# Optimization experiments

Measured on AMD Instinct MI355X. Metric: run time of the kernel, lower is better.

The kernel has to match this reference:

```python
import jax, jax.numpy as jnp
import numpy as np

N_HEADS, D_MODEL, D_HEAD = 16, 1024, 64
BATCH, SEQ = 8, 1024
INIT_RANGE = 0.02
IGNORE = -100000.0


def setup_inputs() -> dict:
    key = jax.random.key(0)
    ks = jax.random.split(key, 6)
    return {
        "normalized_resid_pre": jax.random.normal(ks[0], (BATCH, SEQ, D_MODEL), jnp.float32),
        "encoder_output": jax.random.normal(ks[1], (BATCH, SEQ, D_MODEL), jnp.float32),
        "Qs": jax.random.normal(ks[2], (N_HEADS, D_MODEL, D_HEAD), jnp.float32) * INIT_RANGE,
        "Qbs": jnp.zeros((N_HEADS, D_HEAD), jnp.float32),
        "Ks": jax.random.normal(ks[3], (N_HEADS, D_MODEL, D_HEAD), jnp.float32) * INIT_RANGE,
        "Kbs": jnp.zeros((N_HEADS, D_HEAD), jnp.float32),
        "Vs": jax.random.normal(ks[4], (N_HEADS, D_MODEL, D_HEAD), jnp.float32) * INIT_RANGE,
        "Vbs": jnp.zeros((N_HEADS, D_HEAD), jnp.float32),
        "O": jax.random.normal(ks[5], (N_HEADS, D_HEAD, D_MODEL), jnp.float32) * INIT_RANGE,
        "Ob": jnp.zeros((D_MODEL,), jnp.float32),
    }


def reference(normalized_resid_pre, encoder_output, Qs, Qbs, Ks, Kbs, Vs, Vbs, O, Ob):
    sqrt_d_head = np.sqrt(D_HEAD).astype(np.float32)
    # per-head projections: q,k from encoder_output, v from normalized_resid_pre
    q = jnp.einsum('bpd,hdk->bphk', encoder_output, Qs) + Qbs
    k = jnp.einsum('bpd,hdk->bphk', encoder_output, Ks) + Kbs
    v = jnp.einsum('bpd,hdk->bphk', normalized_resid_pre, Vs) + Vbs
    # [B,H,Q,K] scores, scaled then causally masked with -1e5 (not -inf)
    scores = jnp.einsum('bqhk,bmhk->bhqm', q, k) / sqrt_d_head
    causal = jnp.triu(jnp.ones((SEQ, SEQ), bool), k=1)
    scores = jnp.where(causal, jnp.float32(IGNORE), scores)
    attn = jax.nn.softmax(scores, axis=-1)
    z = jnp.einsum('bmhk,bhqm->bqhk', v, attn)
    return jnp.einsum('bqhk,hkd->bqd', z, O) + Ob
```

## Files before the change

kernel.cpp:

```cpp
#include <hip/hip_runtime.h>
#include <hip/hip_bf16.h>
#include <cstdint>
#include <cstddef>
#include <math.h>


typedef __attribute__((ext_vector_type(8))) short short8;
typedef __attribute__((ext_vector_type(4))) short short4v;
typedef __attribute__((ext_vector_type(4))) float f32x4;

#define MFMA16(A, B, C) __builtin_amdgcn_mfma_f32_16x16x32_bf16(A, B, C, 0, 0, 0)

__device__ inline short f2bs(float f) {
    __bf16 h = (__bf16)f;
    return __builtin_bit_cast(short, h);
}

typedef const __attribute__((address_space(1))) unsigned int* as1_u32p;
typedef __attribute__((address_space(3))) unsigned int* as3_u32p;

__device__ inline void gload_lds16(const void* g, void* lds_base) {
    __builtin_amdgcn_global_load_lds((as1_u32p)(uintptr_t)g,
                                     (as3_u32p)(uintptr_t)lds_base, 16, 0, 0);
}

__global__ __launch_bounds__(256) void cvt_k(const float* __restrict__ a,
                                             const float* __restrict__ b,
                                             short* __restrict__ oa,
                                             short* __restrict__ ob) {
    const int n = 8 * 1024 * 1024;
    const float* src = blockIdx.y ? b : a;
    short* dst = blockIdx.y ? ob : oa;
    for (int i = (blockIdx.x * 256 + threadIdx.x) * 8; i < n; i += gridDim.x * 256 * 8) {
        f32x4 v0 = *(const f32x4*)(src + i), v1 = *(const f32x4*)(src + i + 4);
        short8 o;
        o[0] = f2bs(v0[0]); o[1] = f2bs(v0[1]); o[2] = f2bs(v0[2]); o[3] = f2bs(v0[3]);
        o[4] = f2bs(v1[0]); o[5] = f2bs(v1[1]); o[6] = f2bs(v1[2]); o[7] = f2bs(v1[3]);
        *(short8*)(dst + i) = o;
    }
}

__global__ __launch_bounds__(256) void wtrans_k(
    const float* __restrict__ Wq, const float* __restrict__ Wk,
    const float* __restrict__ Wv, const float* __restrict__ Wo,
    short* __restrict__ TQ, short* __restrict__ TK,
    short* __restrict__ TV, short* __restrict__ TO) {
    __shared__ short tile[64][72];
    const int wsel = blockIdx.y;
    const float* in = wsel == 0 ? Wq : wsel == 1 ? Wk : wsel == 2 ? Wv : Wo;
    short* out = wsel == 0 ? TQ : wsel == 1 ? TK : wsel == 2 ? TV : TO;
    const int h = blockIdx.x >> 4, tk = blockIdx.x & 15;
    const int t = threadIdx.x;
    size_t ioff; int istr, orow0, ocol0;
    if (wsel < 3) { ioff = (size_t)h * 65536 + (size_t)tk * 64 * 64; istr = 64;   orow0 = h * 64;  ocol0 = tk * 64; }
    else          { ioff = (size_t)h * 65536 + (size_t)tk * 64;      istr = 1024; orow0 = tk * 64; ocol0 = h * 64; }
    {
        const int r = t >> 2, c0 = (t & 3) * 16;
        const float* src = in + ioff + (size_t)r * istr + c0;
#pragma unroll
        for (int j = 0; j < 4; j++) {
            f32x4 v = *(const f32x4*)(src + j * 4);
            tile[r][c0 + j * 4 + 0] = f2bs(v[0]);
            tile[r][c0 + j * 4 + 1] = f2bs(v[1]);
            tile[r][c0 + j * 4 + 2] = f2bs(v[2]);
            tile[r][c0 + j * 4 + 3] = f2bs(v[3]);
        }
    }
    __syncthreads();
    {
        const int cc = t >> 2, rb = (t & 3) * 16;
        short8 o0, o1;
#pragma unroll
        for (int j = 0; j < 8; j++) { o0[j] = tile[rb + j][cc]; o1[j] = tile[rb + 8 + j][cc]; }
        short* dst = out + (size_t)(orow0 + cc) * 1024 + ocol0 + rb;
        *(short8*)dst = o0;
        *(short8*)(dst + 8) = o1;
    }
}

template <int MODE>
__global__ __launch_bounds__(256) void gemm_bt(const short* __restrict__ A,
                                               const short* __restrict__ B,
                                               const float* __restrict__ bias,
                                               void* __restrict__ Cp) {
    constexpr int K = 1024;
    __shared__ short As[128 * 64];
    __shared__ short Bs[128 * 64];
    const int t = threadIdx.x, l = t & 63, w = t >> 6, lr = l & 15, lg = l >> 4;
    const int wm = (w >> 1) * 64, wn = (w & 1) * 64;
    const int m0 = blockIdx.x * 128, n0 = blockIdx.y * 128;
    const int sr = l >> 3, cb = l & 7;
    f32x4 acc[4][4] = {};

    for (int k0 = 0; k0 < K; k0 += 64) {
#pragma unroll
        for (int i = 0; i < 4; i++) {
            const int c = w * 4 + i, r = c * 8 + sr, cbs = cb ^ (r & 7);
            gload_lds16(A + (size_t)(m0 + r) * K + k0 + cbs * 8, &As[c * 512]);
        }
#pragma unroll
        for (int i = 0; i < 4; i++) {
            const int c = w * 4 + i, r = c * 8 + sr, cbs = cb ^ (r & 7);
            gload_lds16(B + (size_t)(n0 + r) * K + k0 + cbs * 8, &Bs[c * 512]);
        }
        __syncthreads();
#pragma unroll
        for (int kk = 0; kk < 2; kk++) {
            short8 af[4], bf[4];
#pragma unroll
            for (int mi = 0; mi < 4; mi++) {
                const int r = wm + mi * 16 + lr;
                af[mi] = *(const short8*)&As[r * 64 + ((kk * 4 + lg) ^ (r & 7)) * 8];
            }
#pragma unroll
            for (int nj = 0; nj < 4; nj++) {
                const int r = wn + nj * 16 + lr;
                bf[nj] = *(const short8*)&Bs[r * 64 + ((kk * 4 + lg) ^ (r & 7)) * 8];
            }
#pragma unroll
            for (int mi = 0; mi < 4; mi++)
#pragma unroll
                for (int nj = 0; nj < 4; nj++)
                    acc[mi][nj] = MFMA16(af[mi], bf[nj], acc[mi][nj]);
        }
        __syncthreads();
    }

#pragma unroll
    for (int mi = 0; mi < 4; mi++) {
#pragma unroll
        for (int nj = 0; nj < 4; nj++) {
            const int col = n0 + wn + nj * 16 + lr;
            const float bv = bias[col];
            if (MODE == 2) {
                const int rowb = m0 + wm + mi * 16 + lg * 4;
                const int bb = rowb >> 10, s0 = rowb & 1023;
                const int h = col >> 6, d = col & 63;
                short4v pk;
#pragma unroll
                for (int e = 0; e < 4; e++) pk[e] = f2bs(acc[mi][nj][e] + bv);
                *(short4v*)((short*)Cp + ((size_t)(bb * 16 + h) * 64 + d) * 1024 + s0) = pk;
            } else {
#pragma unroll
                for (int e = 0; e < 4; e++) {
                    const int row = m0 + wm + mi * 16 + lg * 4 + e;
                    const float val = acc[mi][nj][e] + bv;
                    if (MODE == 1) {
                        const int bb = row >> 10, s = row & 1023;
                        const int h = col >> 6, d = col & 63;
                        ((short*)Cp)[((size_t)(bb * 16 + h) * 1024 + s) * 64 + d] = f2bs(val);
                    } else {
                        ((float*)Cp)[(size_t)row * 1024 + col] = val;
                    }
                }
            }
        }
    }
}

#define ATTN_THR 11.5415603f

__device__ __forceinline__ void attn_tile(
    const short* __restrict__ Ks, const short* __restrict__ Vt,
    short (*__restrict__ Psw)[72],
    const short8* __restrict__ qf, float* __restrict__ m,
    float* __restrict__ ps, f32x4* __restrict__ acc,
    bool diag, int lr, int lg, int rowloc) {
    f32x4 sf[4];
#pragma unroll
    for (int n = 0; n < 4; n++) {
        const int rk = n * 16 + lr;
        short8 kf0 = *(const short8*)&Ks[rk * 64 + ((lg) ^ (rk & 7)) * 8];
        short8 kf1 = *(const short8*)&Ks[rk * 64 + ((4 + lg) ^ (rk & 7)) * 8];
        f32x4 s = {};
        s = MFMA16(qf[0], kf0, s);
        s = MFMA16(qf[1], kf1, s);
        sf[n] = s;
    }
    const float SC = 0.18033688f;
#pragma unroll
    for (int n = 0; n < 4; n++)
#pragma unroll
        for (int e = 0; e < 4; e++) {
            float x = sf[n][e] * SC;
            if (diag && (n * 16 + lr > rowloc + e)) x = -1e30f;
            sf[n][e] = x;
        }
    float pm[4];
#pragma unroll
    for (int e = 0; e < 4; e++)
        pm[e] = fmaxf(fmaxf(sf[0][e], sf[1][e]), fmaxf(sf[2][e], sf[3][e]));
    bool ok = true;
#pragma unroll
    for (int e = 0; e < 4; e++) ok = ok && (pm[e] <= m[e] + ATTN_THR);
    if (!__all(ok)) {
#pragma unroll
        for (int e = 0; e < 4; e++) {
            float tm = pm[e];
#pragma unroll
            for (int off = 1; off < 16; off <<= 1)
                tm = fmaxf(tm, __shfl_xor(tm, off));
            float nm = fmaxf(m[e], tm);
            float al = exp2f(m[e] - nm);
            m[e] = nm;
            ps[e] *= al;
#pragma unroll
            for (int n4 = 0; n4 < 4; n4++) acc[n4][e] *= al;
        }
    }
#pragma unroll
    for (int e = 0; e < 4; e++) {
#pragma unroll
        for (int n = 0; n < 4; n++) {
            float p = exp2f(sf[n][e] - m[e]);
            ps[e] += p;
            Psw[lg * 4 + e][n * 16 + lr] = f2bs(p);
        }
    }
#pragma unroll
    for (int c = 0; c < 2; c++) {
        short8 pf = *(const short8*)&Psw[lr][lg * 8 + c * 32];
#pragma unroll
        for (int n4 = 0; n4 < 4; n4++) {
            const int rv = n4 * 16 + lr;
            short8 vf = *(const short8*)&Vt[rv * 64 + ((lg + 4 * c) ^ (rv & 7)) * 8];
            acc[n4] = MFMA16(pf, vf, acc[n4]);
        }
    }
}

__global__ __launch_bounds__(256, 4) void attn_k(const short* __restrict__ Q,
                                                 const short* __restrict__ Kp,
                                                 const short* __restrict__ Vg,
                                                 short* __restrict__ Z) {
    __shared__ short Ks[64 * 64];
    __shared__ short Vt[64 * 64];
    __shared__ short Ps[4][16][72];
    const int t = threadIdx.x, l = t & 63, w = t >> 6, lr = l & 15, lg = l >> 4;
    const int bh = blockIdx.x;
    const int qbA = blockIdx.y, qbB = 15 - qbA;
    const int q0A = qbA * 64, q0B = qbB * 64;
    const size_t base = (size_t)bh * 65536;
    const int sr = l >> 3, cb = l & 7;
    const int rowloc = w * 16 + lg * 4;

    short8 qfA[2], qfB[2];
    {
        const short* qp = Q + base + (size_t)(q0A + w * 16 + lr) * 64 + lg * 8;
        qfA[0] = *(const short8*)qp;
        qfA[1] = *(const short8*)(qp + 32);
        qp = Q + base + (size_t)(q0B + w * 16 + lr) * 64 + lg * 8;
        qfB[0] = *(const short8*)qp;
        qfB[1] = *(const short8*)(qp + 32);
    }

    float mA[4], mB[4], psA[4], psB[4];
    f32x4 accA[4] = {}, accB[4] = {};
#pragma unroll
    for (int e = 0; e < 4; e++) { mA[e] = mB[e] = -1e30f; psA[e] = psB[e] = 0.f; }

    for (int kt = 0; kt <= qbB; kt++) {
        const int k0 = kt * 64;
#pragma unroll
        for (int i = 0; i < 2; i++) {
            const int c = w * 2 + i, r = c * 8 + sr, cbs = cb ^ (r & 7);
            gload_lds16(Kp + base + (size_t)(k0 + r) * 64 + cbs * 8, &Ks[c * 512]);
            gload_lds16(Vg + base + (size_t)r * 1024 + k0 + cbs * 8, &Vt[c * 512]);
        }
        __syncthreads();
        if (kt <= qbA)
            attn_tile(Ks, Vt, Ps[w], qfA, mA, psA, accA, kt == qbA, lr, lg, rowloc);
        attn_tile(Ks, Vt, Ps[w], qfB, mB, psB, accB, kt == qbB, lr, lg, rowloc);
        __syncthreads();
    }

    const int b = bh >> 4, h = bh & 15;
#pragma unroll
    for (int e = 0; e < 4; e++) {
        float sA = psA[e], sB = psB[e];
#pragma unroll
        for (int off = 1; off < 16; off <<= 1) {
            sA += __shfl_xor(sA, off);
            sB += __shfl_xor(sB, off);
        }
        psA[e] = 1.f / sA;
        psB[e] = 1.f / sB;
    }
#pragma unroll
    for (int n4 = 0; n4 < 4; n4++)
#pragma unroll
        for (int e = 0; e < 4; e++) {
            const int rloc = w * 16 + lg * 4 + e;
            Z[((size_t)(b * 1024 + q0A + rloc)) * 1024 + h * 64 + n4 * 16 + lr] =
                f2bs(accA[n4][e] * psA[e]);
            Z[((size_t)(b * 1024 + q0B + rloc)) * 1024 + h * 64 + n4 * 16 + lr] =
                f2bs(accB[n4][e] * psB[e]);
        }
}

extern "C" void kernel_launch(void* const* d_in, const int* in_sizes, int n_in,
                              void* d_out, int out_size, void* d_ws, size_t ws_size,
                              hipStream_t stream) {
    const float* resid = (const float*)d_in[0];
    const float* enc   = (const float*)d_in[1];
    const float* Qs    = (const float*)d_in[2];
    const float* Qbs   = (const float*)d_in[3];
    const float* Ksw   = (const float*)d_in[4];
    const float* Kbs   = (const float*)d_in[5];
    const float* Vs    = (const float*)d_in[6];
    const float* Vbs   = (const float*)d_in[7];
    const float* Ow    = (const float*)d_in[8];
    const float* Ob    = (const float*)d_in[9];
    float* out = (float*)d_out;

    char* ws = (char*)d_ws;
    const size_t M16 = (size_t)16 * 1024 * 1024;
    short* Aenc = (short*)ws;
    short* Ares = (short*)(ws + M16);
    short* Qw   = (short*)(ws + 2 * M16);
    short* Kw   = (short*)(ws + 3 * M16);
    short* Vw   = (short*)(ws + 4 * M16);
    short* WqT  = (short*)(ws + 5 * M16);
    short* WkT  = (short*)(ws + 5 * M16 + 2 * 1024 * 1024);
    short* WvT  = (short*)(ws + 5 * M16 + 4 * 1024 * 1024);
    short* WoT  = (short*)(ws + 5 * M16 + 6 * 1024 * 1024);
    short* Zw   = Aenc;

    cvt_k<<<dim3(2048, 2), 256, 0, stream>>>(enc, resid, Aenc, Ares);
    wtrans_k<<<dim3(256, 4), 256, 0, stream>>>(Qs, Ksw, Vs, Ow, WqT, WkT, WvT, WoT);
    gemm_bt<1><<<dim3(64, 8), 256, 0, stream>>>(Aenc, WqT, Qbs, Qw);
    gemm_bt<1><<<dim3(64, 8), 256, 0, stream>>>(Aenc, WkT, Kbs, Kw);
    gemm_bt<2><<<dim3(64, 8), 256, 0, stream>>>(Ares, WvT, Vbs, Vw);
    attn_k<<<dim3(128, 8), 256, 0, stream>>>(Qw, Kw, Vw, Zw);
    gemm_bt<0><<<dim3(64, 8), 256, 0, stream>>>(Zw, WoT, Ob, out);
}
```

Baseline: 163.5 us.

## Double-buffer K/V tiles in attention and fuse Q/K projection GEMMs

```diff
diff --git a/kernel.cpp b/kernel.cpp
--- a/kernel.cpp
+++ b/kernel.cpp
@@ -82,7 +82,9 @@
 __global__ __launch_bounds__(256) void gemm_bt(const short* __restrict__ A,
                                                const short* __restrict__ B,
                                                const float* __restrict__ bias,
-                                               void* __restrict__ Cp) {
+                                               void* __restrict__ Cp,
+                                               const float* __restrict__ bias2,
+                                               void* __restrict__ Cp2) {
     constexpr int K = 1024;
     __shared__ short As[128 * 64];
     __shared__ short Bs[128 * 64];
@@ -131,8 +133,20 @@
 #pragma unroll
         for (int nj = 0; nj < 4; nj++) {
             const int col = n0 + wn + nj * 16 + lr;
-            const float bv = bias[col];
-            if (MODE == 2) {
+            if (MODE == 3) {
+                const int h2 = col >> 6;
+                short* dst = (short*)(h2 < 16 ? Cp : Cp2);
+                const float bv = h2 < 16 ? bias[col & 1023] : bias2[col & 1023];
+                const int h = h2 & 15, d = col & 63;
+#pragma unroll
+                for (int e = 0; e < 4; e++) {
+                    const int row = m0 + wm + mi * 16 + lg * 4 + e;
+                    const int bb = row >> 10, s = row & 1023;
+                    dst[((size_t)(bb * 16 + h) * 1024 + s) * 64 + d] =
+                        f2bs(acc[mi][nj][e] + bv);
+                }
+            } else if (MODE == 2) {
+                const float bv = bias[col];
                 const int rowb = m0 + wm + mi * 16 + lg * 4;
                 const int bb = rowb >> 10, s0 = rowb & 1023;
                 const int h = col >> 6, d = col & 63;
@@ -141,17 +155,11 @@
                 for (int e = 0; e < 4; e++) pk[e] = f2bs(acc[mi][nj][e] + bv);
                 *(short4v*)((short*)Cp + ((size_t)(bb * 16 + h) * 64 + d) * 1024 + s0) = pk;
             } else {
+                const float bv = bias[col];
 #pragma unroll
                 for (int e = 0; e < 4; e++) {
                     const int row = m0 + wm + mi * 16 + lg * 4 + e;
-                    const float val = acc[mi][nj][e] + bv;
-                    if (MODE == 1) {
-                        const int bb = row >> 10, s = row & 1023;
-                        const int h = col >> 6, d = col & 63;
-                        ((short*)Cp)[((size_t)(bb * 16 + h) * 1024 + s) * 64 + d] = f2bs(val);
-                    } else {
-                        ((float*)Cp)[(size_t)row * 1024 + col] = val;
-                    }
+                    ((float*)Cp)[(size_t)row * 1024 + col] = acc[mi][nj][e] + bv;
                 }
             }
         }
@@ -162,7 +170,7 @@
 
 __device__ __forceinline__ void attn_tile(
     const short* __restrict__ Ks, const short* __restrict__ Vt,
-    short (*__restrict__ Psw)[72],
+    short (*__restrict__ Psw)[76],
     const short8* __restrict__ qf, float* __restrict__ m,
     float* __restrict__ ps, f32x4* __restrict__ acc,
     bool diag, int lr, int lg, int rowloc) {
@@ -229,13 +237,13 @@
     }
 }
 
-__global__ __launch_bounds__(256, 4) void attn_k(const short* __restrict__ Q,
+__global__ __launch_bounds__(256, 3) void attn_k(const short* __restrict__ Q,
                                                  const short* __restrict__ Kp,
                                                  const short* __restrict__ Vg,
                                                  short* __restrict__ Z) {
-    __shared__ short Ks[64 * 64];
-    __shared__ short Vt[64 * 64];
-    __shared__ short Ps[4][16][72];
+    __shared__ short Ks[2][64 * 64];
+    __shared__ short Vt[2][64 * 64];
+    __shared__ short Ps[4][16][76];
     const int t = threadIdx.x, l = t & 63, w = t >> 6, lr = l & 15, lg = l >> 4;
     const int bh = blockIdx.x;
     const int qbA = blockIdx.y, qbB = 15 - qbA;
@@ -259,18 +267,33 @@
 #pragma unroll
     for (int e = 0; e < 4; e++) { mA[e] = mB[e] = -1e30f; psA[e] = psB[e] = 0.f; }
 
+    {
+        const int i0 = w * 2, r0 = i0 * 8 + sr;
+#pragma unroll
+        for (int i = 0; i < 2; i++) {
+            const int c = i0 + i, r = r0 + i * 8, cbs = cb ^ (r & 7);
+            gload_lds16(Kp + base + (size_t)r * 64 + cbs * 8, &Ks[0][c * 512]);
+            gload_lds16(Vg + base + (size_t)r * 1024 + cbs * 8, &Vt[0][c * 512]);
+        }
+    }
+    __syncthreads();
+
     for (int kt = 0; kt <= qbB; kt++) {
-        const int k0 = kt * 64;
-#pragma unroll
-        for (int i = 0; i < 2; i++) {
-            const int c = w * 2 + i, r = c * 8 + sr, cbs = cb ^ (r & 7);
-            gload_lds16(Kp + base + (size_t)(k0 + r) * 64 + cbs * 8, &Ks[c * 512]);
-            gload_lds16(Vg + base + (size_t)r * 1024 + k0 + cbs * 8, &Vt[c * 512]);
-        }
-        __syncthreads();
+        const int cur = kt & 1;
+        if (kt < qbB) {
+            const int k0 = (kt + 1) * 64;
+#pragma unroll
+            for (int i = 0; i < 2; i++) {
+                const int c = w * 2 + i, r = c * 8 + sr, cbs = cb ^ (r & 7);
+                gload_lds16(Kp + base + (size_t)(k0 + r) * 64 + cbs * 8,
+                            &Ks[cur ^ 1][c * 512]);
+                gload_lds16(Vg + base + (size_t)r * 1024 + k0 + cbs * 8,
+                            &Vt[cur ^ 1][c * 512]);
+            }
+        }
         if (kt <= qbA)
-            attn_tile(Ks, Vt, Ps[w], qfA, mA, psA, accA, kt == qbA, lr, lg, rowloc);
-        attn_tile(Ks, Vt, Ps[w], qfB, mB, psB, accB, kt == qbB, lr, lg, rowloc);
+            attn_tile(Ks[cur], Vt[cur], Ps[w], qfA, mA, psA, accA, kt == qbA, lr, lg, rowloc);
+        attn_tile(Ks[cur], Vt[cur], Ps[w], qfB, mB, psB, accB, kt == qbB, lr, lg, rowloc);
         __syncthreads();
     }
 
@@ -328,9 +351,8 @@
 
     cvt_k<<<dim3(2048, 2), 256, 0, stream>>>(enc, resid, Aenc, Ares);
     wtrans_k<<<dim3(256, 4), 256, 0, stream>>>(Qs, Ksw, Vs, Ow, WqT, WkT, WvT, WoT);
-    gemm_bt<1><<<dim3(64, 8), 256, 0, stream>>>(Aenc, WqT, Qbs, Qw);
-    gemm_bt<1><<<dim3(64, 8), 256, 0, stream>>>(Aenc, WkT, Kbs, Kw);
-    gemm_bt<2><<<dim3(64, 8), 256, 0, stream>>>(Ares, WvT, Vbs, Vw);
+    gemm_bt<3><<<dim3(64, 16), 256, 0, stream>>>(Aenc, WqT, Qbs, Qw, Kbs, Kw);
+    gemm_bt<2><<<dim3(64, 8), 256, 0, stream>>>(Ares, WvT, Vbs, Vw, nullptr, nullptr);
     attn_k<<<dim3(128, 8), 256, 0, stream>>>(Qw, Kw, Vw, Zw);
-    gemm_bt<0><<<dim3(64, 8), 256, 0, stream>>>(Zw, WoT, Ob, out);
-}
+    gemm_bt<0><<<dim3(64, 8), 256, 0, stream>>>(Zw, WoT, Ob, out, nullptr, nullptr);
+}
```

Result: slower. 177.2 us (+8.4%).
